# Kernel optimization log

Hardware: AMD Instinct MI355X
Metric: run time of the kernel (lower is better)

Reference implementation:

```python
import jax, jax.numpy as jnp
import numpy as np

L_IN, L_K = 1, 1            # degree ranges (0..L)
C_IN, K_CH, H = 16, 8, 4    # in_channels, k_channels (per head), num_heads
C_OUT = H * K_CH            # 32
E, N_NODES, EMB = 32768, 4096, 64
M_IN, M_K = (L_IN + 1) ** 2, (L_K + 1) ** 2


def _so2_pairs(L_in, L_out):
    # enumerate SO(2)-equivariant weight blocks: for each order m, all (l_in, l_out)
    # pairs with l >= m; m=0 uses 1 matrix, m>0 uses 2 (real/imag parts).
    pairs, w = [], 0
    for m in range(min(L_in, L_out) + 1):
        for l_in in range(m, L_in + 1):
            for l_out in range(m, L_out + 1):
                pairs.append((m, l_in, l_out, w))
                w += 1 if m == 0 else 2
    return pairs, w

_PAIRS, NUM_W = _so2_pairs(L_IN, L_K)  # NUM_W = 6 for L_in=L_k=1


def so2_linear(x, W, L_in, L_out):
    # x: [E, (L_in+1)^2, Cin]; W: [NUM_W, Cin, Cout] (shared) or [E, NUM_W, Cin, Cout] (per-edge)
    per_edge = (W.ndim == 4)
    Cout = W.shape[-1]
    out = jnp.zeros((x.shape[0], (L_out + 1) ** 2, Cout), x.dtype)

    def mat(xs, w):
        return jnp.einsum('ec,eco->eo', xs, W[:, w]) if per_edge else xs @ W[w]

    pairs, _ = _so2_pairs(L_in, L_out)
    for m, l_in, l_out, w in pairs:
        i_in, i_out = l_in * (l_in + 1), l_out * (l_out + 1)  # flat index of (l, m=0)
        if m == 0:
            out = out.at[:, i_out].add(mat(x[:, i_in], w))
        else:
            xp, xn = x[:, i_in + m], x[:, i_in - m]
            out = out.at[:, i_out + m].add(mat(xp, w) - mat(xn, w + 1))
            out = out.at[:, i_out - m].add(mat(xp, w + 1) + mat(xn, w))
    return out


def segment_softmax(z, index, num_segments):
    # PyG-style softmax over ragged neighborhoods (max is detached, as in PyG)
    zmax = jax.lax.stop_gradient(jax.ops.segment_max(z, index, num_segments=num_segments))
    e = jnp.exp(z - zmax[index])
    denom = jax.ops.segment_sum(e, index, num_segments=num_segments)
    return e / denom[index]


def setup_inputs() -> dict:
    key = jax.random.key(0)
    ks = jax.random.split(key, 6)
    x_q = jax.random.normal(ks[0], (E, M_IN, C_IN), jnp.float32)
    x_k = jax.random.normal(ks[1], (E, M_IN, C_IN), jnp.float32)
    edge_emb = jax.random.normal(ks[2], (E, EMB), jnp.float32)
    index = jnp.sort(jax.random.randint(ks[3], (E,), 0, N_NODES))
    W_q = jax.random.normal(ks[4], (NUM_W, C_IN, C_OUT), jnp.float32) / np.sqrt(C_IN)
    W_p = jax.random.normal(ks[5], (EMB, NUM_W * C_IN * C_OUT), jnp.float32) / np.sqrt(EMB)
    return {"x_q": x_q, "x_k": x_k, "edge_emb": edge_emb, "index": index,
            "W_q": W_q, "W_p": W_p, "num_nodes": N_NODES}


def reference(x_q, x_k, edge_emb, index, W_q, W_p, num_nodes):
    # q_ij = W_Q x_i ; static SO2 weights
    q = so2_linear(x_q, W_q, L_IN, L_K).reshape(-1, M_K, H, K_CH)
    # k_ij = W_K(||r_ij||) x_j ; per-edge dynamic SO2 weights from edge embedding
    W_k = (edge_emb @ W_p).reshape(-1, NUM_W, C_IN, C_OUT)
    k = so2_linear(x_k, W_k, L_IN, L_K).reshape(-1, M_K, H, K_CH)
    scale = (K_CH // H) ** (-0.5)  # faithful to original: (k_channels // num_heads)**-0.5
    z = (q * k).sum((-1, -3)) * scale  # [E, H]
    return segment_softmax(z, index, num_nodes)
```

## Files before the change

kernel.cpp:

```cpp
#include <hip/hip_runtime.h>
#include <math.h>

#define E_TOTAL 32768
#define NUM_NODES 4096
#define SCALE 0.70710678118654752f

typedef __attribute__((ext_vector_type(8))) short bfrag;
typedef __attribute__((ext_vector_type(16))) float facc;

__device__ inline unsigned short f2bf(float f) {
  unsigned int u = __float_as_uint(f);
  unsigned int r = (u + 0x7FFFu + ((u >> 16) & 1u)) >> 16;
  return (unsigned short)r;
}
__device__ inline float bf2f(unsigned short s) {
  return __uint_as_float(((unsigned int)s) << 16);
}
__device__ inline void cvt8(const float* v, bfrag& hi, bfrag& lo) {
#pragma unroll
  for (int i = 0; i < 8; ++i) {
    unsigned short h = f2bf(v[i]);
    hi[i] = (short)h;
    lo[i] = (short)f2bf(v[i] - bf2f(h));
  }
}

__device__ inline void stage16(const void* g, void* l) {
  __builtin_amdgcn_global_load_lds(
      (const __attribute__((address_space(1))) unsigned int*)g,
      (__attribute__((address_space(3))) unsigned int*)l, 16, 0, 0);
}

__global__ __launch_bounds__(256) void prep_kernel(
    const float* __restrict__ Wp, const float* __restrict__ Wq,
    const int* __restrict__ index,
    unsigned short* __restrict__ fragWp, unsigned short* __restrict__ fragWq,
    int* __restrict__ offs)
{
  const int b = blockIdx.x, t = threadIdx.x;
  if (b < 96) {
    __shared__ unsigned short lds[4096];
    const int c = b / 6, w = b - c * 6;
    const int colbase = w * 512 + c * 32;
    const int cl = t & 31, dg = t >> 5;
#pragma unroll
    for (int i = 0; i < 8; ++i) {
      const int d = dg * 8 + i;
      const float v = Wp[(size_t)d * 3072 + colbase + cl];
      const unsigned short hi = f2bf(v);
      const unsigned short lo = f2bf(v - bf2f(hi));
      const int ks = d >> 4;
      const int lane = ((d >> 3) & 1) * 32 + cl;
      const int j = d & 7;
      lds[(ks * 2 + 0) * 512 + lane * 8 + j] = hi;
      lds[(ks * 2 + 1) * 512 + lane * 8 + j] = lo;
    }
    __syncthreads();
    unsigned short* dst = fragWp + (size_t)b * 4096;
    ((uint4*)dst)[t] = ((const uint4*)lds)[t];
    ((uint4*)dst)[t + 256] = ((const uint4*)lds)[t + 256];
  } else if (b < 103) {
    const int slot = b - 96;
    const int w = (slot == 6) ? 5 : slot;
    const float sgn = (slot == 6) ? -1.f : 1.f;
    for (int tt = t; tt < 512; tt += 256) {
      const int lane = tt >> 3, j = tt & 7;
      const int o = lane & 31, c = (lane >> 5) * 8 + j;
      const float v = sgn * Wq[(size_t)(w * 16 + c) * 32 + o];
      const unsigned short hi = f2bf(v);
      const unsigned short lo = f2bf(v - bf2f(hi));
      fragWq[slot * 1024 + lane * 8 + j] = hi;
      fragWq[slot * 1024 + 512 + lane * 8 + j] = lo;
    }
  } else {
    const int tg = (b - 103) * 256 + t;
    if (tg >= E_TOTAL) return;
    const int cur = index[tg];
    const int prev = (tg == 0) ? -1 : index[tg - 1];
    for (int n = prev + 1; n <= cur; ++n) offs[n] = tg;
    if (tg == E_TOTAL - 1)
      for (int n = cur + 1; n <= NUM_NODES; ++n) offs[n] = E_TOTAL;
  }
}

__global__ __launch_bounds__(256, 1) void main_kernel(
    const float* __restrict__ x_q, const float* __restrict__ x_k,
    const float* __restrict__ emb,
    const unsigned short* __restrict__ fragWp,
    const unsigned short* __restrict__ fragWq,
    float* __restrict__ z)
{
  __shared__ float xk_t[64][129];
  __shared__ alignas(16) unsigned short wbuf[2][4096];

  const int t = threadIdx.x;
  const int lane = t & 63, wv = t >> 6;
  const int col = lane & 31, half = lane >> 5;
  const int eb = blockIdx.x * 128;
  const int el = wv * 32 + col;
  const int e = eb + el;

  {
    const int er = t & 127, dh = (t >> 7) * 32;
    const float* src = x_k + (size_t)(eb + er) * 64 + dh;
#pragma unroll
    for (int i = 0; i < 8; ++i) {
      float4 v = *(const float4*)(src + i * 4);
      xk_t[dh + i * 4 + 0][er] = v.x;
      xk_t[dh + i * 4 + 1][er] = v.y;
      xk_t[dh + i * 4 + 2][er] = v.z;
      xk_t[dh + i * 4 + 3][er] = v.w;
    }
  }

  {
    const char* tb = (const char*)fragWp;
    char* db = (char*)&wbuf[0][0];
    stage16(tb + (wv * 2 + 0) * 1024 + lane * 16, db + (wv * 2 + 0) * 1024);
    stage16(tb + (wv * 2 + 1) * 1024 + lane * 16, db + (wv * 2 + 1) * 1024);
  }

  bfrag ebh[4], ebl[4];
#pragma unroll
  for (int ks = 0; ks < 4; ++ks) {
    float tmp[8];
    *(float4*)&tmp[0] = *(const float4*)(emb + (size_t)e * 64 + ks * 16 + half * 8);
    *(float4*)&tmp[4] = *(const float4*)(emb + (size_t)e * 64 + ks * 16 + half * 8 + 4);
    cvt8(tmp, ebh[ks], ebl[ks]);
  }

  facc ka0 = {0}, ka1 = {0}, ka2 = {0}, ka3 = {0};

  __syncthreads();

  float xkc0 = 0.f, xkc1 = 0.f, xkc2 = 0.f, xkc3 = 0.f;

  for (int ot = 0; ot < 16; ++ot) {
#pragma unroll
    for (int ii = 0; ii < 6; ++ii) {
      const int it = ot * 6 + ii;
      if (it != 95) {
        const char* tb = (const char*)fragWp + (size_t)(it + 1) * 8192;
        char* db = (char*)&wbuf[(ii + 1) & 1][0];
        stage16(tb + (wv * 2 + 0) * 1024 + lane * 16, db + (wv * 2 + 0) * 1024);
        stage16(tb + (wv * 2 + 1) * 1024 + lane * 16, db + (wv * 2 + 1) * 1024);
      }
      if (ii == 0) {
        xkc0 = xk_t[ot][el];
        xkc1 = xk_t[16 + ot][el];
        xkc2 = xk_t[32 + ot][el];
        xkc3 = xk_t[48 + ot][el];
      }
      const unsigned short* wb = &wbuf[ii & 1][0];
      bfrag ch[4], cl4[4];
#pragma unroll
      for (int ks = 0; ks < 4; ++ks) {
        *(uint4*)&ch[ks]  = *(const uint4*)(wb + ks * 1024 + lane * 8);
        *(uint4*)&cl4[ks] = *(const uint4*)(wb + ks * 1024 + 512 + lane * 8);
      }
      facc cc0 = {0.f}, cc1 = {0.f}, cc2 = {0.f};
#pragma unroll
      for (int ks = 0; ks < 4; ++ks) {
        cc0 = __builtin_amdgcn_mfma_f32_32x32x16_bf16(ch[ks], ebh[ks], cc0, 0, 0, 0);
        cc1 = __builtin_amdgcn_mfma_f32_32x32x16_bf16(ch[ks], ebl[ks], cc1, 0, 0, 0);
        cc2 = __builtin_amdgcn_mfma_f32_32x32x16_bf16(cl4[ks], ebh[ks], cc2, 0, 0, 0);
      }
      if (ii < 4) {
        const float xv = (ii & 2) ? xkc2 : xkc0;
        facc& kd = (ii & 1) ? ka2 : ka0;
#pragma unroll
        for (int r = 0; r < 16; ++r)
          kd[r] = fmaf(xv, cc0[r] + cc1[r] + cc2[r], kd[r]);
      } else if (ii == 4) {
#pragma unroll
        for (int r = 0; r < 16; ++r) {
          const float s = cc0[r] + cc1[r] + cc2[r];
          ka1[r] = fmaf(xkc1, s, ka1[r]);
          ka3[r] = fmaf(xkc3, s, ka3[r]);
        }
      } else {
#pragma unroll
        for (int r = 0; r < 16; ++r) {
          const float s = cc0[r] + cc1[r] + cc2[r];
          ka1[r] = fmaf(xkc3, s, ka1[r]);
          ka3[r] = fmaf(-xkc1, s, ka3[r]);
        }
      }
      __syncthreads();
    }
  }

  bfrag xqh[4], xql[4];
#pragma unroll
  for (int a = 0; a < 4; ++a) {
    float tmp[8];
    *(float4*)&tmp[0] = *(const float4*)(x_q + (size_t)e * 64 + a * 16 + half * 8);
    *(float4*)&tmp[4] = *(const float4*)(x_q + (size_t)e * 64 + a * 16 + half * 8 + 4);
    cvt8(tmp, xqh[a], xql[a]);
  }
  float zp0 = 0.f, zp1 = 0.f, zp2 = 0.f, zp3 = 0.f;
  const int QA1[4] = {0, 1, 0, 3}, QS1[4] = {0, 4, 1, 4};
  const int QA2[4] = {2, 3, 2, 1}, QS2[4] = {2, 5, 3, 6};
#pragma unroll
  for (int m = 0; m < 4; ++m) {
    facc qa = {0.f};
#pragma unroll
    for (int tm = 0; tm < 2; ++tm) {
      const int a = tm ? QA2[m] : QA1[m];
      const int sl = tm ? QS2[m] : QS1[m];
      bfrag wh, wl;
      *(uint4*)&wh = *(const uint4*)(fragWq + sl * 1024 + lane * 8);
      *(uint4*)&wl = *(const uint4*)(fragWq + sl * 1024 + 512 + lane * 8);
      qa = __builtin_amdgcn_mfma_f32_32x32x16_bf16(wh, xqh[a], qa, 0, 0, 0);
      qa = __builtin_amdgcn_mfma_f32_32x32x16_bf16(wh, xql[a], qa, 0, 0, 0);
      qa = __builtin_amdgcn_mfma_f32_32x32x16_bf16(wl, xqh[a], qa, 0, 0, 0);
    }
    const facc& km = (m == 0) ? ka0 : (m == 1) ? ka1 : (m == 2) ? ka2 : ka3;
#pragma unroll
    for (int r = 0; r < 16; ++r) {
      const float v = qa[r] * km[r];
      if (r < 4) zp0 += v;
      else if (r < 8) zp1 += v;
      else if (r < 12) zp2 += v;
      else zp3 += v;
    }
  }
  zp0 += __shfl_xor(zp0, 32);
  zp1 += __shfl_xor(zp1, 32);
  zp2 += __shfl_xor(zp2, 32);
  zp3 += __shfl_xor(zp3, 32);
  if (half == 0) {
    float4 v = {zp0 * SCALE, zp1 * SCALE, zp2 * SCALE, zp3 * SCALE};
    *(float4*)&z[(size_t)e * 4] = v;
  }
}

__global__ __launch_bounds__(256) void softmax_kernel(
    const float* __restrict__ z, const int* __restrict__ offs,
    float* __restrict__ out)
{
  const int node = blockIdx.x * 4 + (threadIdx.x >> 6);
  const int lane = threadIdx.x & 63;
  const int start = offs[node], end = offs[node + 1];
  if (start >= end) return;
  const int h = lane & 3, eo = lane >> 2;
  float m = -INFINITY;
  for (int e = start + eo; e < end; e += 16) m = fmaxf(m, z[(size_t)e * 4 + h]);
#pragma unroll
  for (int s = 4; s < 64; s <<= 1) m = fmaxf(m, __shfl_xor(m, s));
  float sum = 0.f;
  for (int e = start + eo; e < end; e += 16) sum += __expf(z[(size_t)e * 4 + h] - m);
#pragma unroll
  for (int s = 4; s < 64; s <<= 1) sum += __shfl_xor(sum, s);
  const float inv = 1.f / sum;
  for (int e = start + eo; e < end; e += 16)
    out[(size_t)e * 4 + h] = __expf(z[(size_t)e * 4 + h] - m) * inv;
}

extern "C" void kernel_launch(void* const* d_in, const int* in_sizes, int n_in,
                              void* d_out, int out_size, void* d_ws, size_t ws_size,
                              hipStream_t stream) {
  const float* x_q = (const float*)d_in[0];
  const float* x_k = (const float*)d_in[1];
  const float* emb = (const float*)d_in[2];
  const int* index = (const int*)d_in[3];
  const float* W_q = (const float*)d_in[4];
  const float* W_p = (const float*)d_in[5];
  float* out = (float*)d_out;

  char* ws = (char*)d_ws;
  float* z = (float*)ws;
  int* offs = (int*)(ws + 524288);
  unsigned short* fragWp = (unsigned short*)(ws + 524288 + 32768);
  unsigned short* fragWq = (unsigned short*)(ws + 524288 + 32768 + 786432);

  prep_kernel<<<231, 256, 0, stream>>>(W_p, W_q, index, fragWp, fragWq, offs);
  main_kernel<<<256, 256, 0, stream>>>(x_q, x_k, emb, fragWp, fragWq, z);
  softmax_kernel<<<1024, 256, 0, stream>>>(z, offs, out);
}
```

Before: 145.9 us.

## Deepen W_p staging to four LDS buffers and register-prefetch MFMA fragments

```diff
diff --git a/kernel.cpp b/kernel.cpp
--- a/kernel.cpp
+++ b/kernel.cpp
@@ -91,7 +91,7 @@
     float* __restrict__ z)
 {
   __shared__ float xk_t[64][129];
-  __shared__ alignas(16) unsigned short wbuf[2][4096];
+  __shared__ alignas(16) unsigned short wbuf[4][4096];
 
   const int t = threadIdx.x;
   const int lane = t & 63, wv = t >> 6;
@@ -100,6 +100,14 @@
   const int el = wv * 32 + col;
   const int e = eb + el;
 
+#pragma unroll
+  for (int pt = 0; pt < 3; ++pt) {
+    const char* tb = (const char*)fragWp + (size_t)pt * 8192;
+    char* db = (char*)&wbuf[pt][0];
+    stage16(tb + (wv * 2 + 0) * 1024 + lane * 16, db + (wv * 2 + 0) * 1024);
+    stage16(tb + (wv * 2 + 1) * 1024 + lane * 16, db + (wv * 2 + 1) * 1024);
+  }
+
   {
     const int er = t & 127, dh = (t >> 7) * 32;
     const float* src = x_k + (size_t)(eb + er) * 64 + dh;
@@ -113,13 +121,6 @@
     }
   }
 
-  {
-    const char* tb = (const char*)fragWp;
-    char* db = (char*)&wbuf[0][0];
-    stage16(tb + (wv * 2 + 0) * 1024 + lane * 16, db + (wv * 2 + 0) * 1024);
-    stage16(tb + (wv * 2 + 1) * 1024 + lane * 16, db + (wv * 2 + 1) * 1024);
-  }
-
   bfrag ebh[4], ebl[4];
 #pragma unroll
   for (int ks = 0; ks < 4; ++ks) {
@@ -133,62 +134,103 @@
 
   __syncthreads();
 
+  bfrag fA[8], fB[8];
+  {
+    const unsigned short* wb = &wbuf[0][0] + lane * 8;
+#pragma unroll
+    for (int ks = 0; ks < 4; ++ks) {
+      *(uint4*)&fA[ks]     = *(const uint4*)(wb + ks * 1024);
+      *(uint4*)&fA[ks + 4] = *(const uint4*)(wb + ks * 1024 + 512);
+    }
+  }
+
   float xkc0 = 0.f, xkc1 = 0.f, xkc2 = 0.f, xkc3 = 0.f;
 
-  for (int ot = 0; ot < 16; ++ot) {
-#pragma unroll
-    for (int ii = 0; ii < 6; ++ii) {
-      const int it = ot * 6 + ii;
-      if (it != 95) {
-        const char* tb = (const char*)fragWp + (size_t)(it + 1) * 8192;
-        char* db = (char*)&wbuf[(ii + 1) & 1][0];
-        stage16(tb + (wv * 2 + 0) * 1024 + lane * 16, db + (wv * 2 + 0) * 1024);
-        stage16(tb + (wv * 2 + 1) * 1024 + lane * 16, db + (wv * 2 + 1) * 1024);
-      }
-      if (ii == 0) {
-        xkc0 = xk_t[ot][el];
-        xkc1 = xk_t[16 + ot][el];
-        xkc2 = xk_t[32 + ot][el];
-        xkc3 = xk_t[48 + ot][el];
-      }
-      const unsigned short* wb = &wbuf[ii & 1][0];
-      bfrag ch[4], cl4[4];
-#pragma unroll
-      for (int ks = 0; ks < 4; ++ks) {
-        *(uint4*)&ch[ks]  = *(const uint4*)(wb + ks * 1024 + lane * 8);
-        *(uint4*)&cl4[ks] = *(const uint4*)(wb + ks * 1024 + 512 + lane * 8);
-      }
-      facc cc0 = {0.f}, cc1 = {0.f}, cc2 = {0.f};
-#pragma unroll
-      for (int ks = 0; ks < 4; ++ks) {
-        cc0 = __builtin_amdgcn_mfma_f32_32x32x16_bf16(ch[ks], ebh[ks], cc0, 0, 0, 0);
-        cc1 = __builtin_amdgcn_mfma_f32_32x32x16_bf16(ch[ks], ebl[ks], cc1, 0, 0, 0);
-        cc2 = __builtin_amdgcn_mfma_f32_32x32x16_bf16(cl4[ks], ebh[ks], cc2, 0, 0, 0);
-      }
-      if (ii < 4) {
-        const float xv = (ii & 2) ? xkc2 : xkc0;
-        facc& kd = (ii & 1) ? ka2 : ka0;
-#pragma unroll
-        for (int r = 0; r < 16; ++r)
-          kd[r] = fmaf(xv, cc0[r] + cc1[r] + cc2[r], kd[r]);
-      } else if (ii == 4) {
-#pragma unroll
-        for (int r = 0; r < 16; ++r) {
-          const float s = cc0[r] + cc1[r] + cc2[r];
-          ka1[r] = fmaf(xkc1, s, ka1[r]);
-          ka3[r] = fmaf(xkc3, s, ka3[r]);
-        }
-      } else {
-#pragma unroll
-        for (int r = 0; r < 16; ++r) {
-          const float s = cc0[r] + cc1[r] + cc2[r];
-          ka1[r] = fmaf(xkc3, s, ka1[r]);
-          ka3[r] = fmaf(-xkc1, s, ka3[r]);
-        }
-      }
-      __syncthreads();
-    }
-  }
+#define PHASE(IT, II, DO_STAGE, VMN_STR, DO_NEXT)                              \
+  {                                                                            \
+    if (DO_STAGE) {                                                            \
+      const char* tb = (const char*)fragWp + (size_t)((IT) + 3) * 8192;        \
+      char* db = (char*)&wbuf[((II) + 3) & 3][0];                              \
+      stage16(tb + (wv * 2 + 0) * 1024 + lane * 16, db + (wv * 2 + 0) * 1024); \
+      stage16(tb + (wv * 2 + 1) * 1024 + lane * 16, db + (wv * 2 + 1) * 1024); \
+    }                                                                          \
+    asm volatile("s_waitcnt vmcnt(" VMN_STR ") lgkmcnt(0)" ::: "memory");      \
+    __builtin_amdgcn_s_barrier();                                              \
+    asm volatile("" ::: "memory");                                             \
+    if (((II) % 6) == 0) {                                                     \
+      const int c16 = (IT) / 6;                                                \
+      xkc0 = xk_t[c16][el];      xkc1 = xk_t[16 + c16][el];                    \
+      xkc2 = xk_t[32 + c16][el]; xkc3 = xk_t[48 + c16][el];                    \
+    }                                                                          \
+    bfrag* curf = (((II) & 1) == 0) ? fA : fB;                                 \
+    bfrag* nxtf = (((II) & 1) == 0) ? fB : fA;                                 \
+    if (DO_NEXT) {                                                             \
+      const unsigned short* wb = &wbuf[((II) + 1) & 3][0] + lane * 8;          \
+      _Pragma("unroll")                                                        \
+      for (int ks = 0; ks < 4; ++ks) {                                         \
+        *(uint4*)&nxtf[ks]     = *(const uint4*)(wb + ks * 1024);              \
+        *(uint4*)&nxtf[ks + 4] = *(const uint4*)(wb + ks * 1024 + 512);        \
+      }                                                                        \
+    }                                                                          \
+    facc cc0 = {0.f}, cc1 = {0.f}, cc2 = {0.f};                                \
+    _Pragma("unroll")                                                          \
+    for (int ks = 0; ks < 4; ++ks) {                                           \
+      cc0 = __builtin_amdgcn_mfma_f32_32x32x16_bf16(curf[ks], ebh[ks], cc0, 0, 0, 0);     \
+      cc1 = __builtin_amdgcn_mfma_f32_32x32x16_bf16(curf[ks], ebl[ks], cc1, 0, 0, 0);     \
+      cc2 = __builtin_amdgcn_mfma_f32_32x32x16_bf16(curf[ks + 4], ebh[ks], cc2, 0, 0, 0); \
+    }                                                                          \
+    const int W = (II) % 6;                                                    \
+    if (W < 4) {                                                               \
+      const float xv = (W & 2) ? xkc2 : xkc0;                                  \
+      facc& kd = (W & 1) ? ka2 : ka0;                                          \
+      _Pragma("unroll")                                                        \
+      for (int r = 0; r < 16; ++r)                                             \
+        kd[r] = fmaf(xv, cc0[r] + cc1[r] + cc2[r], kd[r]);                     \
+    } else if (W == 4) {                                                       \
+      _Pragma("unroll")                                                        \
+      for (int r = 0; r < 16; ++r) {                                           \
+        const float s = cc0[r] + cc1[r] + cc2[r];                              \
+        ka1[r] = fmaf(xkc1, s, ka1[r]);                                        \
+        ka3[r] = fmaf(xkc3, s, ka3[r]);                                        \
+      }                                                                        \
+    } else {                                                                   \
+      _Pragma("unroll")                                                        \
+      for (int r = 0; r < 16; ++r) {                                           \
+        const float s = cc0[r] + cc1[r] + cc2[r];                              \
+        ka1[r] = fmaf(xkc3, s, ka1[r]);                                        \
+        ka3[r] = fmaf(-xkc1, s, ka3[r]);                                       \
+      }                                                                        \
+    }                                                                          \
+  }
+
+  for (int ot = 0; ot < 7; ++ot) {
+    const int base = ot * 12;
+    PHASE(base + 0,  0,  true, "4", true)
+    PHASE(base + 1,  1,  true, "4", true)
+    PHASE(base + 2,  2,  true, "4", true)
+    PHASE(base + 3,  3,  true, "4", true)
+    PHASE(base + 4,  4,  true, "4", true)
+    PHASE(base + 5,  5,  true, "4", true)
+    PHASE(base + 6,  6,  true, "4", true)
+    PHASE(base + 7,  7,  true, "4", true)
+    PHASE(base + 8,  8,  true, "4", true)
+    PHASE(base + 9,  9,  true, "4", true)
+    PHASE(base + 10, 10, true, "4", true)
+    PHASE(base + 11, 11, true, "4", true)
+  }
+  PHASE(84, 0,  true,  "4", true)
+  PHASE(85, 1,  true,  "4", true)
+  PHASE(86, 2,  true,  "4", true)
+  PHASE(87, 3,  true,  "4", true)
+  PHASE(88, 4,  true,  "4", true)
+  PHASE(89, 5,  true,  "4", true)
+  PHASE(90, 6,  true,  "4", true)
+  PHASE(91, 7,  true,  "4", true)
+  PHASE(92, 8,  true,  "4", true)
+  PHASE(93, 9,  false, "2", true)
+  PHASE(94, 10, false, "0", true)
+  PHASE(95, 11, false, "0", false)
+#undef PHASE
 
   bfrag xqh[4], xql[4];
 #pragma unroll
```

New measurement: 164.0 us. +12.4%, slower.
